# Kernel tuning notes

Hardware: AMD Instinct MI355X
Metric: run time of the kernel (lower is better)

## Reference

```python
import jax, jax.numpy as jnp
import numpy as np

N_NODES = 50000
N_EDGES = 800000
DIM = 128
NUM_GRAPHS = 512
NEG_SLOPE_ATT = 0.2   # GATConv attention leaky_relu slope
NEG_SLOPE_ACT = 0.01  # F.leaky_relu default in forward
EPS = 1e-16


def setup_inputs() -> dict:
    key = jax.random.key(0)
    ks = jax.random.split(key, 10)
    x = jax.random.normal(ks[0], (N_NODES, DIM), dtype=jnp.float32)
    edge_index = jax.random.randint(ks[1], (2, N_EDGES), 0, N_NODES, dtype=jnp.int64)
    batch = jnp.sort(jax.random.randint(ks[2], (N_NODES,), 0, NUM_GRAPHS, dtype=jnp.int64))
    s = 1.0 / np.sqrt(DIM)
    inp = {"x": x, "edge_index": edge_index, "batch": batch}
    for i in range(3):
        inp[f"W{i}"] = jax.random.uniform(ks[3 + i], (DIM, DIM), jnp.float32, -s, s)
        a = jax.random.uniform(ks[6 + i], (2, DIM), jnp.float32, -s, s)
        inp[f"a_src{i}"] = a[0]
        inp[f"a_dst{i}"] = a[1]
    return inp


def _gat_conv(x, src, dst, W, a_src, a_dst):
    # h = lin(x); heads=1, concat, bias=False
    h = x @ W.T                                     # [N, D]
    e = jax.nn.leaky_relu((h @ a_src)[src] + (h @ a_dst)[dst], NEG_SLOPE_ATT)  # [E]
    # segment softmax over destination neighborhoods
    m = jax.ops.segment_max(e, dst, num_segments=N_NODES)
    ee = jnp.exp(e - m[dst])
    z = jax.ops.segment_sum(ee, dst, num_segments=N_NODES)
    alpha = ee / (z[dst] + EPS)                     # [E]
    return jax.ops.segment_sum(h[src] * alpha[:, None], dst, num_segments=N_NODES)


def reference(x, edge_index, batch, W0, a_src0, a_dst0, W1, a_src1, a_dst1, W2, a_src2, a_dst2):
    loops = jnp.arange(N_NODES, dtype=edge_index.dtype)
    src = jnp.concatenate([edge_index[0], loops])  # add_self_loops=True
    dst = jnp.concatenate([edge_index[1], loops])
    x = _gat_conv(x, src, dst, W0, a_src0, a_dst0)
    x = _gat_conv(x, src, dst, W1, a_src1, a_dst1)
    x = jax.nn.leaky_relu(x, NEG_SLOPE_ACT)
    x = _gat_conv(x, src, dst, W2, a_src2, a_dst2)
    # global_add_pool
    return jax.ops.segment_sum(x, batch, num_segments=NUM_GRAPHS)
```

## Files before the change

kernel.cpp:

```cpp
#include <hip/hip_runtime.h>
#include <hip/hip_bf16.h>
#include <hip/hip_fp16.h>
#include <math.h>

#define NN 50000
#define NE 800000
#define DD 128
#define NG 512
#define NSA 0.2f
#define NSB 0.01f
#define EPS 1e-16f
#define CAP 61

typedef _Float16 half8 __attribute__((ext_vector_type(8)));
typedef float    floatx4 __attribute__((ext_vector_type(4)));

__global__ void init_kernel(unsigned short* __restrict__ csr_p, float* __restrict__ out,
                            const float* __restrict__ W0, const float* __restrict__ W1,
                            const float* __restrict__ W2, __half* __restrict__ w16) {
    int i = blockIdx.x * 256 + threadIdx.x;
    if (i < NN) ((unsigned int*)csr_p)[(size_t)i << 5] = 0;
    if (i < NG * DD) out[i] = 0.f;
    if (i < 3 * DD * DD) {
        int layer = i / (DD * DD), idx = i % (DD * DD);
        const float* Ws = (layer == 0) ? W0 : (layer == 1) ? W1 : W2;
        w16[i] = __float2half(Ws[idx]);
    }
}

#define BM 64
__device__ __forceinline__ void gemm_mfma_body(
        const float* __restrict__ X, const __half* __restrict__ W16,
        const float* __restrict__ a_src, const float* __restrict__ a_dst,
        __half* __restrict__ H16, float* __restrict__ as_, float* __restrict__ ad_,
        int row0, __half (*tile)[136]) {
    int t    = threadIdx.x;
    int wave = t >> 6;
    int lane = t & 63;
    int quad = lane >> 4;
    int mrow = lane & 15;
    int gl = min(row0 + wave * 16 + mrow, NN - 1);

    half8 afrag[4];
    #pragma unroll
    for (int kc = 0; kc < 4; ++kc) {
        int k = kc * 32 + quad * 8;
        float4 u0 = *(const float4*)&X[(size_t)gl * DD + k];
        float4 u1 = *(const float4*)&X[(size_t)gl * DD + k + 4];
        half8 a;
        a[0] = (_Float16)u0.x; a[1] = (_Float16)u0.y;
        a[2] = (_Float16)u0.z; a[3] = (_Float16)u0.w;
        a[4] = (_Float16)u1.x; a[5] = (_Float16)u1.y;
        a[6] = (_Float16)u1.z; a[7] = (_Float16)u1.w;
        afrag[kc] = a;
    }

    floatx4 acc[8] = {};
    #pragma unroll
    for (int ct = 0; ct < 8; ++ct) {
        #pragma unroll
        for (int kc = 0; kc < 4; ++kc) {
            half8 b = *(const half8*)&W16[(size_t)(ct * 16 + mrow) * DD + kc * 32 + quad * 8];
            acc[ct] = __builtin_amdgcn_mfma_f32_16x16x32_f16(afrag[kc], b, acc[ct], 0, 0, 0);
        }
    }
    #pragma unroll
    for (int ct = 0; ct < 8; ++ct) {
        #pragma unroll
        for (int reg = 0; reg < 4; ++reg)
            tile[wave * 16 + quad * 4 + reg][ct * 16 + mrow] = __float2half(acc[ct][reg]);
    }
    __syncthreads();

    int tx = t & 15;
    int ty = t >> 4;
    float asv[8], adv[8];
    #pragma unroll
    for (int c = 0; c < 8; ++c) {
        asv[c] = a_src[tx * 8 + c];
        adv[c] = a_dst[tx * 8 + c];
    }
    #pragma unroll
    for (int r = 0; r < 4; ++r) {
        int row = ty * 4 + r;
        int gr = row0 + row;
        float4 raw = *(const float4*)&tile[row][tx * 8];
        const __half2* q = (const __half2*)&raw;
        float2 c01 = __half22float2(q[0]);
        float2 c23 = __half22float2(q[1]);
        float2 c45 = __half22float2(q[2]);
        float2 c67 = __half22float2(q[3]);
        float hv[8] = {c01.x, c01.y, c23.x, c23.y, c45.x, c45.y, c67.x, c67.y};
        float ps = 0.f, pd = 0.f;
        #pragma unroll
        for (int c = 0; c < 8; ++c) {
            ps += hv[c] * asv[c];
            pd += hv[c] * adv[c];
        }
        #pragma unroll
        for (int off = 8; off >= 1; off >>= 1) {
            ps += __shfl_xor(ps, off);
            pd += __shfl_xor(pd, off);
        }
        if (gr < NN) {
            if (tx == 0) { as_[gr] = ps; ad_[gr] = pd; }
            *(float4*)&H16[(size_t)gr * DD + tx * 8] = raw;
        }
    }
}

__global__ __launch_bounds__(256, 4) void fat_kernel(
        int gemm_nblocks,
        const float* __restrict__ X, const __half* __restrict__ W16,
        const float* __restrict__ a_src, const float* __restrict__ a_dst,
        __half* __restrict__ H16, float* __restrict__ as_, float* __restrict__ ad_,
        const int* __restrict__ esrc, const int* __restrict__ edst,
        unsigned short* __restrict__ csr_p) {
    __shared__ __half tile[BM][136];
    if ((int)blockIdx.x >= gemm_nblocks) {
        int i = (blockIdx.x - gemm_nblocks) * 256 + threadIdx.x;
        if (i < NE / 8) {
            int4 sa = ((const int4*)esrc)[i * 2];
            int4 sb = ((const int4*)esrc)[i * 2 + 1];
            int4 da = ((const int4*)edst)[i * 2];
            int4 db = ((const int4*)edst)[i * 2 + 1];
            int k0 = atomicAdd((unsigned int*)&csr_p[(size_t)da.x << 6], 1u);
            int k1 = atomicAdd((unsigned int*)&csr_p[(size_t)da.y << 6], 1u);
            int k2 = atomicAdd((unsigned int*)&csr_p[(size_t)da.z << 6], 1u);
            int k3 = atomicAdd((unsigned int*)&csr_p[(size_t)da.w << 6], 1u);
            int k4 = atomicAdd((unsigned int*)&csr_p[(size_t)db.x << 6], 1u);
            int k5 = atomicAdd((unsigned int*)&csr_p[(size_t)db.y << 6], 1u);
            int k6 = atomicAdd((unsigned int*)&csr_p[(size_t)db.z << 6], 1u);
            int k7 = atomicAdd((unsigned int*)&csr_p[(size_t)db.w << 6], 1u);
            if (k0 < CAP) csr_p[((size_t)da.x << 6) + 2 + k0] = (unsigned short)sa.x;
            if (k1 < CAP) csr_p[((size_t)da.y << 6) + 2 + k1] = (unsigned short)sa.y;
            if (k2 < CAP) csr_p[((size_t)da.z << 6) + 2 + k2] = (unsigned short)sa.z;
            if (k3 < CAP) csr_p[((size_t)da.w << 6) + 2 + k3] = (unsigned short)sa.w;
            if (k4 < CAP) csr_p[((size_t)db.x << 6) + 2 + k4] = (unsigned short)sb.x;
            if (k5 < CAP) csr_p[((size_t)db.y << 6) + 2 + k5] = (unsigned short)sb.y;
            if (k6 < CAP) csr_p[((size_t)db.z << 6) + 2 + k6] = (unsigned short)sb.z;
            if (k7 < CAP) csr_p[((size_t)db.w << 6) + 2 + k7] = (unsigned short)sb.w;
        }
        return;
    }
    gemm_mfma_body(X, W16, a_src, a_dst, H16, as_, ad_, blockIdx.x * BM, tile);
}

__device__ inline void xr4s(float4& a, int off) {
    a.x += __shfl_xor(a.x, off);
    a.y += __shfl_xor(a.y, off);
    a.z += __shfl_xor(a.z, off);
    a.w += __shfl_xor(a.w, off);
}
__device__ inline void fma_h8(float4& a0, float4& a1, float p, const float4& raw) {
    const __half2* q = (const __half2*)&raw;
    float2 c;
    c = __half22float2(q[0]); a0.x += p * c.x; a0.y += p * c.y;
    c = __half22float2(q[1]); a0.z += p * c.x; a0.w += p * c.y;
    c = __half22float2(q[2]); a1.x += p * c.x; a1.y += p * c.y;
    c = __half22float2(q[3]); a1.z += p * c.x; a1.w += p * c.y;
}

__device__ __forceinline__ void agg_batch4(
        int row0, int wid, int lane,
        const __half* __restrict__ H16, const float* __restrict__ as_,
        const float* __restrict__ ad_, const unsigned short* __restrict__ csr_p,
        float (*p_sh)[4][64], int (*s_sh)[4][64], __half (*ytile)[136],
        int apply_lrelu) {
    int nodes[4], deg[4], sv[4];
    float adn[4], ll[4];

    int cnt[4];
    #pragma unroll
    for (int it = 0; it < 4; ++it) {
        nodes[it] = row0 + it * 4 + wid;
        cnt[it] = (int)*(const unsigned int*)&csr_p[(size_t)nodes[it] << 6];
    }
    int sl[4];
    #pragma unroll
    for (int it = 0; it < 4; ++it)
        sl[it] = (int)csr_p[((size_t)nodes[it] << 6) + 2 + lane];
    #pragma unroll
    for (int it = 0; it < 4; ++it) adn[it] = ad_[nodes[it]];
    #pragma unroll
    for (int it = 0; it < 4; ++it) {
        int dr = min(cnt[it], CAP);
        deg[it] = dr + 1;
        sv[it] = (lane < dr) ? sl[it] : nodes[it];
        s_sh[wid][it][lane] = sv[it];
    }
    float av[4];
    #pragma unroll
    for (int it = 0; it < 4; ++it) av[it] = as_[sv[it]];
    #pragma unroll
    for (int it = 0; it < 4; ++it) {
        float e = -1e30f;
        if (lane < deg[it]) {
            float ev = av[it] + adn[it];
            e = (ev > 0.f) ? ev : NSA * ev;
        }
        float m = e;
        #pragma unroll
        for (int off = 32; off >= 1; off >>= 1) m = fmaxf(m, __shfl_xor(m, off));
        float pv = (lane < deg[it]) ? __expf(e - m) : 0.f;
        p_sh[wid][it][lane] = pv;
        float l = pv;
        #pragma unroll
        for (int off = 32; off >= 1; off >>= 1) l += __shfl_xor(l, off);
        ll[it] = l;
    }
    __builtin_amdgcn_wave_barrier();

    int g = lane >> 4;
    int d = lane & 15;
    const float4* H4 = (const float4*)H16;
    #pragma unroll
    for (int it = 0; it < 4; ++it) {
        int degp = (deg[it] + 15) & ~15;
        float4 a0 = {0,0,0,0}, a1 = {0,0,0,0};
        for (int j = g; j < degp; j += 16) {
            int   sa = s_sh[wid][it][j];
            int   sb = s_sh[wid][it][j + 4];
            int   sc = s_sh[wid][it][j + 8];
            int   sd = s_sh[wid][it][j + 12];
            float pa = p_sh[wid][it][j];
            float pb = p_sh[wid][it][j + 4];
            float pc = p_sh[wid][it][j + 8];
            float pd = p_sh[wid][it][j + 12];
            float4 ra = H4[(size_t)sa * 16 + d];
            float4 rb = H4[(size_t)sb * 16 + d];
            float4 rc = H4[(size_t)sc * 16 + d];
            float4 rd = H4[(size_t)sd * 16 + d];
            fma_h8(a0, a1, pa, ra);
            fma_h8(a0, a1, pb, rb);
            fma_h8(a0, a1, pc, rc);
            fma_h8(a0, a1, pd, rd);
        }
        xr4s(a0, 16); xr4s(a0, 32);
        xr4s(a1, 16); xr4s(a1, 32);
        if (g == 0) {
            float inv = 1.f / (ll[it] + EPS);
            float4 o0, o1;
            o0.x = a0.x * inv; o0.y = a0.y * inv; o0.z = a0.z * inv; o0.w = a0.w * inv;
            o1.x = a1.x * inv; o1.y = a1.y * inv; o1.z = a1.z * inv; o1.w = a1.w * inv;
            if (apply_lrelu) {
                o0.x = (o0.x > 0.f) ? o0.x : NSB * o0.x;
                o0.y = (o0.y > 0.f) ? o0.y : NSB * o0.y;
                o0.z = (o0.z > 0.f) ? o0.z : NSB * o0.z;
                o0.w = (o0.w > 0.f) ? o0.w : NSB * o0.w;
                o1.x = (o1.x > 0.f) ? o1.x : NSB * o1.x;
                o1.y = (o1.y > 0.f) ? o1.y : NSB * o1.y;
                o1.z = (o1.z > 0.f) ? o1.z : NSB * o1.z;
                o1.w = (o1.w > 0.f) ? o1.w : NSB * o1.w;
            }
            __half2 hh[4];
            hh[0] = __floats2half2_rn(o0.x, o0.y);
            hh[1] = __floats2half2_rn(o0.z, o0.w);
            hh[2] = __floats2half2_rn(o1.x, o1.y);
            hh[3] = __floats2half2_rn(o1.z, o1.w);
            *(float4*)&ytile[it * 4 + wid][d * 8] = *(float4*)hh;
        }
    }
}

__global__ __launch_bounds__(256, 6) void agg_gemm_kernel(
        const __half* __restrict__ H_in, const float* __restrict__ as_in,
        const float* __restrict__ ad_in, const unsigned short* __restrict__ csr_p,
        const __half* __restrict__ W16, const float* __restrict__ a_src,
        const float* __restrict__ a_dst, __half* __restrict__ H_out,
        float* __restrict__ as_out, float* __restrict__ ad_out, int apply_lrelu) {
    __shared__ float  p_sh[4][4][64];
    __shared__ int    s_sh[4][4][64];
    __shared__ __half ytile[16][136];
    int t = threadIdx.x;
    int wid = t >> 6, lane = t & 63;
    int row0 = blockIdx.x * 16;

    agg_batch4(row0, wid, lane, H_in, as_in, ad_in, csr_p, p_sh, s_sh, ytile,
               apply_lrelu);
    __syncthreads();

    int quad = lane >> 4, mrow = lane & 15;
    half8 afrag[4];
    #pragma unroll
    for (int kc = 0; kc < 4; ++kc)
        afrag[kc] = *(const half8*)&ytile[mrow][kc * 32 + quad * 8];
    __syncthreads();

    floatx4 acc[2] = {};
    #pragma unroll
    for (int cc = 0; cc < 2; ++cc) {
        int ct = wid * 2 + cc;
        #pragma unroll
        for (int kc = 0; kc < 4; ++kc) {
            half8 b = *(const half8*)&W16[(size_t)(ct * 16 + mrow) * DD + kc * 32 + quad * 8];
            acc[cc] = __builtin_amdgcn_mfma_f32_16x16x32_f16(afrag[kc], b, acc[cc], 0, 0, 0);
        }
    }
    #pragma unroll
    for (int cc = 0; cc < 2; ++cc) {
        int ct = wid * 2 + cc;
        #pragma unroll
        for (int reg = 0; reg < 4; ++reg)
            ytile[quad * 4 + reg][ct * 16 + mrow] = __float2half(acc[cc][reg]);
    }
    __syncthreads();

    int row = t >> 4, cg = t & 15;
    int gr = row0 + row;
    float4 raw = *(const float4*)&ytile[row][cg * 8];
    const __half2* q = (const __half2*)&raw;
    float2 c01 = __half22float2(q[0]);
    float2 c23 = __half22float2(q[1]);
    float2 c45 = __half22float2(q[2]);
    float2 c67 = __half22float2(q[3]);
    float hv[8] = {c01.x, c01.y, c23.x, c23.y, c45.x, c45.y, c67.x, c67.y};
    float ps = 0.f, pd = 0.f;
    #pragma unroll
    for (int c = 0; c < 8; ++c) {
        ps += hv[c] * a_src[cg * 8 + c];
        pd += hv[c] * a_dst[cg * 8 + c];
    }
    #pragma unroll
    for (int off = 8; off >= 1; off >>= 1) {
        ps += __shfl_xor(ps, off);
        pd += __shfl_xor(pd, off);
    }
    if (cg == 0) { as_out[gr] = ps; ad_out[gr] = pd; }
    *(float4*)&H_out[(size_t)gr * DD + cg * 8] = raw;
}

__global__ __launch_bounds__(256, 6) void agg_pool_kernel(
        const __half* __restrict__ H_in, const float* __restrict__ as_in,
        const float* __restrict__ ad_in, const unsigned short* __restrict__ csr_p,
        const int* __restrict__ batch, float* __restrict__ out) {
    __shared__ float  p_sh[4][4][64];
    __shared__ int    s_sh[4][4][64];
    __shared__ __half ytile[16][136];
    int t = threadIdx.x;
    int wid = t >> 6, lane = t & 63;
    int row0 = blockIdx.x * 16;

    agg_batch4(row0, wid, lane, H_in, as_in, ad_in, csr_p, p_sh, s_sh, ytile, 0);
    __syncthreads();

    int rh = t >> 7;
    int d  = t & 127;
    int r0 = rh * 8;
    float acc = 0.f;
    int g = batch[row0 + r0];
    #pragma unroll
    for (int r = 0; r < 8; ++r) {
        int n = row0 + r0 + r;
        int gn = batch[n];
        if (gn != g) {
            atomicAdd(&out[(size_t)g * DD + d], acc);
            acc = 0.f;
            g = gn;
        }
        acc += __half2float(ytile[r0 + r][d]);
    }
    atomicAdd(&out[(size_t)g * DD + d], acc);
}

extern "C" void kernel_launch(void* const* d_in, const int* in_sizes, int n_in,
                              void* d_out, int out_size, void* d_ws, size_t ws_size,
                              hipStream_t stream) {
    const float* x      = (const float*)d_in[0];
    const int*   ei     = (const int*)d_in[1];
    const int*   batch  = (const int*)d_in[2];
    const int*   src    = ei;
    const int*   dst    = ei + NE;
    float* out = (float*)d_out;

    size_t off = 0;
    auto carve = [&](size_t bytes) {
        void* p = (char*)d_ws + off;
        off += (bytes + 255) & ~(size_t)255;
        return p;
    };
    __half* h16a  = (__half*)carve((size_t)NN * DD * 2);
    __half* h16b  = (__half*)carve((size_t)NN * DD * 2);
    float*  as_a  = (float*)carve((size_t)NN * 4);
    float*  ad_a  = (float*)carve((size_t)NN * 4);
    float*  as_b  = (float*)carve((size_t)NN * 4);
    float*  ad_b  = (float*)carve((size_t)NN * 4);
    unsigned short* csr_p = (unsigned short*)carve((size_t)NN * 64 * 2);
    __half* w16   = (__half*)carve((size_t)3 * DD * DD * 2);

    const int gemm_blocks = (NN + BM - 1) / BM;
    const int scat_blocks = (NE / 8 + 255) / 256;
    const int fuse_blocks = NN / 16;
    const int init_blocks = (NN * 16 + 255) / 256;

    const float* W0  = (const float*)d_in[3];
    const float* av0 = (const float*)d_in[4];
    const float* ad0 = (const float*)d_in[5];
    const float* av1 = (const float*)d_in[7];
    const float* ad1 = (const float*)d_in[8];
    const float* av2 = (const float*)d_in[10];
    const float* ad2 = (const float*)d_in[11];

    init_kernel<<<init_blocks, 256, 0, stream>>>(csr_p, out, W0,
                                                 (const float*)d_in[6],
                                                 (const float*)d_in[9], w16);
    fat_kernel<<<gemm_blocks + scat_blocks, 256, 0, stream>>>(
        gemm_blocks, x, w16, av0, ad0, h16a, as_a, ad_a, src, dst, csr_p);

    agg_gemm_kernel<<<fuse_blocks, 256, 0, stream>>>(
        h16a, as_a, ad_a, csr_p, w16 + (size_t)1 * DD * DD, av1, ad1,
        h16b, as_b, ad_b, 0);
    agg_gemm_kernel<<<fuse_blocks, 256, 0, stream>>>(
        h16b, as_b, ad_b, csr_p, w16 + (size_t)2 * DD * DD, av2, ad2,
        h16a, as_a, ad_a, 1);

    agg_pool_kernel<<<fuse_blocks, 256, 0, stream>>>(h16a, as_a, ad_a, csr_p,
                                                     batch, out);
}
```

Baseline: 252.5 us.

## Give each 16-lane group its own node in aggregation and split CSR counters

Aggregation is reorganized so each 16-lane group of a wave processes one destination node over its whole neighbor list with 8 gathers in flight. This replaces four groups cooperating on each node and then combining partials with xor shuffles. Edge counts move out of the padded CSR rows into a separate counter array with one counter per 64 bytes. The edge scatter now handles 4 edges per thread and its blocks are interleaved with the GEMM blocks of the first kernel. Launch bounds for the aggregation kernels drop from 6 to 4. The trade-off is more load imbalance between groups whose nodes have different degrees, and possibly lower occupancy.

```diff
diff --git a/kernel.cpp b/kernel.cpp
--- a/kernel.cpp
+++ b/kernel.cpp
@@ -15,11 +15,11 @@
 typedef _Float16 half8 __attribute__((ext_vector_type(8)));
 typedef float    floatx4 __attribute__((ext_vector_type(4)));
 
-__global__ void init_kernel(unsigned short* __restrict__ csr_p, float* __restrict__ out,
+__global__ void init_kernel(unsigned int* __restrict__ cnt, float* __restrict__ out,
                             const float* __restrict__ W0, const float* __restrict__ W1,
                             const float* __restrict__ W2, __half* __restrict__ w16) {
     int i = blockIdx.x * 256 + threadIdx.x;
-    if (i < NN) ((unsigned int*)csr_p)[(size_t)i << 5] = 0;
+    if (i < NN) cnt[(size_t)i << 4] = 0u;
     if (i < NG * DD) out[i] = 0.f;
     if (i < 3 * DD * DD) {
         int layer = i / (DD * DD), idx = i % (DD * DD);
@@ -110,48 +110,32 @@
 }
 
 __global__ __launch_bounds__(256, 4) void fat_kernel(
-        int gemm_nblocks,
         const float* __restrict__ X, const __half* __restrict__ W16,
         const float* __restrict__ a_src, const float* __restrict__ a_dst,
         __half* __restrict__ H16, float* __restrict__ as_, float* __restrict__ ad_,
         const int* __restrict__ esrc, const int* __restrict__ edst,
-        unsigned short* __restrict__ csr_p) {
+        unsigned int* __restrict__ cnt, unsigned short* __restrict__ slots) {
     __shared__ __half tile[BM][136];
-    if ((int)blockIdx.x >= gemm_nblocks) {
-        int i = (blockIdx.x - gemm_nblocks) * 256 + threadIdx.x;
-        if (i < NE / 8) {
-            int4 sa = ((const int4*)esrc)[i * 2];
-            int4 sb = ((const int4*)esrc)[i * 2 + 1];
-            int4 da = ((const int4*)edst)[i * 2];
-            int4 db = ((const int4*)edst)[i * 2 + 1];
-            int k0 = atomicAdd((unsigned int*)&csr_p[(size_t)da.x << 6], 1u);
-            int k1 = atomicAdd((unsigned int*)&csr_p[(size_t)da.y << 6], 1u);
-            int k2 = atomicAdd((unsigned int*)&csr_p[(size_t)da.z << 6], 1u);
-            int k3 = atomicAdd((unsigned int*)&csr_p[(size_t)da.w << 6], 1u);
-            int k4 = atomicAdd((unsigned int*)&csr_p[(size_t)db.x << 6], 1u);
-            int k5 = atomicAdd((unsigned int*)&csr_p[(size_t)db.y << 6], 1u);
-            int k6 = atomicAdd((unsigned int*)&csr_p[(size_t)db.z << 6], 1u);
-            int k7 = atomicAdd((unsigned int*)&csr_p[(size_t)db.w << 6], 1u);
-            if (k0 < CAP) csr_p[((size_t)da.x << 6) + 2 + k0] = (unsigned short)sa.x;
-            if (k1 < CAP) csr_p[((size_t)da.y << 6) + 2 + k1] = (unsigned short)sa.y;
-            if (k2 < CAP) csr_p[((size_t)da.z << 6) + 2 + k2] = (unsigned short)sa.z;
-            if (k3 < CAP) csr_p[((size_t)da.w << 6) + 2 + k3] = (unsigned short)sa.w;
-            if (k4 < CAP) csr_p[((size_t)db.x << 6) + 2 + k4] = (unsigned short)sb.x;
-            if (k5 < CAP) csr_p[((size_t)db.y << 6) + 2 + k5] = (unsigned short)sb.y;
-            if (k6 < CAP) csr_p[((size_t)db.z << 6) + 2 + k6] = (unsigned short)sb.z;
-            if (k7 < CAP) csr_p[((size_t)db.w << 6) + 2 + k7] = (unsigned short)sb.w;
+    int bx = blockIdx.x;
+    if (bx & 1) {
+        int i = (bx >> 1) * 256 + threadIdx.x;
+        if (i < NE / 4) {
+            int4 s4 = ((const int4*)esrc)[i];
+            int4 d4 = ((const int4*)edst)[i];
+            int k0 = (int)atomicAdd(&cnt[(size_t)d4.x << 4], 1u);
+            int k1 = (int)atomicAdd(&cnt[(size_t)d4.y << 4], 1u);
+            int k2 = (int)atomicAdd(&cnt[(size_t)d4.z << 4], 1u);
+            int k3 = (int)atomicAdd(&cnt[(size_t)d4.w << 4], 1u);
+            if (k0 < CAP) slots[((size_t)d4.x << 6) + k0] = (unsigned short)s4.x;
+            if (k1 < CAP) slots[((size_t)d4.y << 6) + k1] = (unsigned short)s4.y;
+            if (k2 < CAP) slots[((size_t)d4.z << 6) + k2] = (unsigned short)s4.z;
+            if (k3 < CAP) slots[((size_t)d4.w << 6) + k3] = (unsigned short)s4.w;
         }
         return;
     }
-    gemm_mfma_body(X, W16, a_src, a_dst, H16, as_, ad_, blockIdx.x * BM, tile);
-}
-
-__device__ inline void xr4s(float4& a, int off) {
-    a.x += __shfl_xor(a.x, off);
-    a.y += __shfl_xor(a.y, off);
-    a.z += __shfl_xor(a.z, off);
-    a.w += __shfl_xor(a.w, off);
-}
+    gemm_mfma_body(X, W16, a_src, a_dst, H16, as_, ad_, (bx >> 1) * BM, tile);
+}
+
 __device__ inline void fma_h8(float4& a0, float4& a1, float p, const float4& raw) {
     const __half2* q = (const __half2*)&raw;
     float2 c;
@@ -164,34 +148,36 @@
 __device__ __forceinline__ void agg_batch4(
         int row0, int wid, int lane,
         const __half* __restrict__ H16, const float* __restrict__ as_,
-        const float* __restrict__ ad_, const unsigned short* __restrict__ csr_p,
+        const float* __restrict__ ad_, const unsigned int* __restrict__ cnt,
+        const unsigned short* __restrict__ slots,
         float (*p_sh)[4][64], int (*s_sh)[4][64], __half (*ytile)[136],
         int apply_lrelu) {
-    int nodes[4], deg[4], sv[4];
+    int nodes[4], deg[4];
     float adn[4], ll[4];
 
-    int cnt[4];
+    int cv[4];
     #pragma unroll
     for (int it = 0; it < 4; ++it) {
         nodes[it] = row0 + it * 4 + wid;
-        cnt[it] = (int)*(const unsigned int*)&csr_p[(size_t)nodes[it] << 6];
+        cv[it] = (int)cnt[(size_t)nodes[it] << 4];
     }
     int sl[4];
     #pragma unroll
     for (int it = 0; it < 4; ++it)
-        sl[it] = (int)csr_p[((size_t)nodes[it] << 6) + 2 + lane];
+        sl[it] = (int)slots[((size_t)nodes[it] << 6) + lane];
     #pragma unroll
     for (int it = 0; it < 4; ++it) adn[it] = ad_[nodes[it]];
+    int svv[4];
     #pragma unroll
     for (int it = 0; it < 4; ++it) {
-        int dr = min(cnt[it], CAP);
+        int dr = min(cv[it], CAP);
         deg[it] = dr + 1;
-        sv[it] = (lane < dr) ? sl[it] : nodes[it];
-        s_sh[wid][it][lane] = sv[it];
+        svv[it] = (lane < dr) ? sl[it] : nodes[it];
+        s_sh[wid][it][lane] = svv[it];
     }
     float av[4];
     #pragma unroll
-    for (int it = 0; it < 4; ++it) av[it] = as_[sv[it]];
+    for (int it = 0; it < 4; ++it) av[it] = as_[svv[it]];
     #pragma unroll
     for (int it = 0; it < 4; ++it) {
         float e = -1e30f;
@@ -213,59 +199,61 @@
 
     int g = lane >> 4;
     int d = lane & 15;
-    const float4* H4 = (const float4*)H16;
-    #pragma unroll
-    for (int it = 0; it < 4; ++it) {
-        int degp = (deg[it] + 15) & ~15;
-        float4 a0 = {0,0,0,0}, a1 = {0,0,0,0};
-        for (int j = g; j < degp; j += 16) {
-            int   sa = s_sh[wid][it][j];
-            int   sb = s_sh[wid][it][j + 4];
-            int   sc = s_sh[wid][it][j + 8];
-            int   sd = s_sh[wid][it][j + 12];
-            float pa = p_sh[wid][it][j];
-            float pb = p_sh[wid][it][j + 4];
-            float pc = p_sh[wid][it][j + 8];
-            float pd = p_sh[wid][it][j + 12];
-            float4 ra = H4[(size_t)sa * 16 + d];
-            float4 rb = H4[(size_t)sb * 16 + d];
-            float4 rc = H4[(size_t)sc * 16 + d];
-            float4 rd = H4[(size_t)sd * 16 + d];
-            fma_h8(a0, a1, pa, ra);
-            fma_h8(a0, a1, pb, rb);
-            fma_h8(a0, a1, pc, rc);
-            fma_h8(a0, a1, pd, rd);
-        }
-        xr4s(a0, 16); xr4s(a0, 32);
-        xr4s(a1, 16); xr4s(a1, 32);
-        if (g == 0) {
-            float inv = 1.f / (ll[it] + EPS);
-            float4 o0, o1;
-            o0.x = a0.x * inv; o0.y = a0.y * inv; o0.z = a0.z * inv; o0.w = a0.w * inv;
-            o1.x = a1.x * inv; o1.y = a1.y * inv; o1.z = a1.z * inv; o1.w = a1.w * inv;
-            if (apply_lrelu) {
-                o0.x = (o0.x > 0.f) ? o0.x : NSB * o0.x;
-                o0.y = (o0.y > 0.f) ? o0.y : NSB * o0.y;
-                o0.z = (o0.z > 0.f) ? o0.z : NSB * o0.z;
-                o0.w = (o0.w > 0.f) ? o0.w : NSB * o0.w;
-                o1.x = (o1.x > 0.f) ? o1.x : NSB * o1.x;
-                o1.y = (o1.y > 0.f) ? o1.y : NSB * o1.y;
-                o1.z = (o1.z > 0.f) ? o1.z : NSB * o1.z;
-                o1.w = (o1.w > 0.f) ? o1.w : NSB * o1.w;
-            }
-            __half2 hh[4];
-            hh[0] = __floats2half2_rn(o0.x, o0.y);
-            hh[1] = __floats2half2_rn(o0.z, o0.w);
-            hh[2] = __floats2half2_rn(o1.x, o1.y);
-            hh[3] = __floats2half2_rn(o1.z, o1.w);
-            *(float4*)&ytile[it * 4 + wid][d * 8] = *(float4*)hh;
-        }
-    }
-}
-
-__global__ __launch_bounds__(256, 6) void agg_gemm_kernel(
+    int   dg = (g == 0) ? deg[0] : (g == 1) ? deg[1] : (g == 2) ? deg[2] : deg[3];
+    float lg = (g == 0) ? ll[0]  : (g == 1) ? ll[1]  : (g == 2) ? ll[2]  : ll[3];
+    const int*    srow = s_sh[wid][g];
+    const float*  prow = p_sh[wid][g];
+    const float4* H4   = (const float4*)H16;
+    float4 a0 = {0,0,0,0}, a1 = {0,0,0,0};
+    int degp = (dg + 7) & ~7;
+    for (int j = 0; j < degp; j += 8) {
+        int s0 = srow[j+0], s1 = srow[j+1], s2 = srow[j+2], s3 = srow[j+3];
+        int s4 = srow[j+4], s5 = srow[j+5], s6 = srow[j+6], s7 = srow[j+7];
+        float p0 = prow[j+0], p1 = prow[j+1], p2 = prow[j+2], p3 = prow[j+3];
+        float p4 = prow[j+4], p5 = prow[j+5], p6 = prow[j+6], p7 = prow[j+7];
+        float4 r0 = H4[(size_t)s0 * 16 + d];
+        float4 r1 = H4[(size_t)s1 * 16 + d];
+        float4 r2 = H4[(size_t)s2 * 16 + d];
+        float4 r3 = H4[(size_t)s3 * 16 + d];
+        float4 r4 = H4[(size_t)s4 * 16 + d];
+        float4 r5 = H4[(size_t)s5 * 16 + d];
+        float4 r6 = H4[(size_t)s6 * 16 + d];
+        float4 r7 = H4[(size_t)s7 * 16 + d];
+        fma_h8(a0, a1, p0, r0);
+        fma_h8(a0, a1, p1, r1);
+        fma_h8(a0, a1, p2, r2);
+        fma_h8(a0, a1, p3, r3);
+        fma_h8(a0, a1, p4, r4);
+        fma_h8(a0, a1, p5, r5);
+        fma_h8(a0, a1, p6, r6);
+        fma_h8(a0, a1, p7, r7);
+    }
+    float inv = 1.f / (lg + EPS);
+    float4 o0, o1;
+    o0.x = a0.x * inv; o0.y = a0.y * inv; o0.z = a0.z * inv; o0.w = a0.w * inv;
+    o1.x = a1.x * inv; o1.y = a1.y * inv; o1.z = a1.z * inv; o1.w = a1.w * inv;
+    if (apply_lrelu) {
+        o0.x = (o0.x > 0.f) ? o0.x : NSB * o0.x;
+        o0.y = (o0.y > 0.f) ? o0.y : NSB * o0.y;
+        o0.z = (o0.z > 0.f) ? o0.z : NSB * o0.z;
+        o0.w = (o0.w > 0.f) ? o0.w : NSB * o0.w;
+        o1.x = (o1.x > 0.f) ? o1.x : NSB * o1.x;
+        o1.y = (o1.y > 0.f) ? o1.y : NSB * o1.y;
+        o1.z = (o1.z > 0.f) ? o1.z : NSB * o1.z;
+        o1.w = (o1.w > 0.f) ? o1.w : NSB * o1.w;
+    }
+    __half2 hh[4];
+    hh[0] = __floats2half2_rn(o0.x, o0.y);
+    hh[1] = __floats2half2_rn(o0.z, o0.w);
+    hh[2] = __floats2half2_rn(o1.x, o1.y);
+    hh[3] = __floats2half2_rn(o1.z, o1.w);
+    *(float4*)&ytile[g * 4 + wid][d * 8] = *(float4*)hh;
+}
+
+__global__ __launch_bounds__(256, 4) void agg_gemm_kernel(
         const __half* __restrict__ H_in, const float* __restrict__ as_in,
-        const float* __restrict__ ad_in, const unsigned short* __restrict__ csr_p,
+        const float* __restrict__ ad_in, const unsigned int* __restrict__ cnt,
+        const unsigned short* __restrict__ slots,
         const __half* __restrict__ W16, const float* __restrict__ a_src,
         const float* __restrict__ a_dst, __half* __restrict__ H_out,
         float* __restrict__ as_out, float* __restrict__ ad_out, int apply_lrelu) {
@@ -276,7 +264,7 @@
     int wid = t >> 6, lane = t & 63;
     int row0 = blockIdx.x * 16;
 
-    agg_batch4(row0, wid, lane, H_in, as_in, ad_in, csr_p, p_sh, s_sh, ytile,
+    agg_batch4(row0, wid, lane, H_in, as_in, ad_in, cnt, slots, p_sh, s_sh, ytile,
                apply_lrelu);
     __syncthreads();
 
@@ -330,9 +318,10 @@
     *(float4*)&H_out[(size_t)gr * DD + cg * 8] = raw;
 }
 
-__global__ __launch_bounds__(256, 6) void agg_pool_kernel(
+__global__ __launch_bounds__(256, 4) void agg_pool_kernel(
         const __half* __restrict__ H_in, const float* __restrict__ as_in,
-        const float* __restrict__ ad_in, const unsigned short* __restrict__ csr_p,
+        const float* __restrict__ ad_in, const unsigned int* __restrict__ cnt,
+        const unsigned short* __restrict__ slots,
         const int* __restrict__ batch, float* __restrict__ out) {
     __shared__ float  p_sh[4][4][64];
     __shared__ int    s_sh[4][4][64];
@@ -341,7 +330,7 @@
     int wid = t >> 6, lane = t & 63;
     int row0 = blockIdx.x * 16;
 
-    agg_batch4(row0, wid, lane, H_in, as_in, ad_in, csr_p, p_sh, s_sh, ytile, 0);
+    agg_batch4(row0, wid, lane, H_in, as_in, ad_in, cnt, slots, p_sh, s_sh, ytile, 0);
     __syncthreads();
 
     int rh = t >> 7;
@@ -385,13 +374,14 @@
     float*  ad_a  = (float*)carve((size_t)NN * 4);
     float*  as_b  = (float*)carve((size_t)NN * 4);
     float*  ad_b  = (float*)carve((size_t)NN * 4);
-    unsigned short* csr_p = (unsigned short*)carve((size_t)NN * 64 * 2);
+    unsigned int*   cnt   = (unsigned int*)carve((size_t)NN * 16 * 4);
+    unsigned short* slots = (unsigned short*)carve((size_t)NN * 64 * 2);
     __half* w16   = (__half*)carve((size_t)3 * DD * DD * 2);
 
     const int gemm_blocks = (NN + BM - 1) / BM;
-    const int scat_blocks = (NE / 8 + 255) / 256;
+    const int fat_blocks  = gemm_blocks * 2;
     const int fuse_blocks = NN / 16;
-    const int init_blocks = (NN * 16 + 255) / 256;
+    const int init_blocks = (NG * DD + 255) / 256;
 
     const float* W0  = (const float*)d_in[3];
     const float* av0 = (const float*)d_in[4];
@@ -401,19 +391,19 @@
     const float* av2 = (const float*)d_in[10];
     const float* ad2 = (const float*)d_in[11];
 
-    init_kernel<<<init_blocks, 256, 0, stream>>>(csr_p, out, W0,
+    init_kernel<<<init_blocks, 256, 0, stream>>>(cnt, out, W0,
                                                  (const float*)d_in[6],
                                                  (const float*)d_in[9], w16);
-    fat_kernel<<<gemm_blocks + scat_blocks, 256, 0, stream>>>(
-        gemm_blocks, x, w16, av0, ad0, h16a, as_a, ad_a, src, dst, csr_p);
+    fat_kernel<<<fat_blocks, 256, 0, stream>>>(
+        x, w16, av0, ad0, h16a, as_a, ad_a, src, dst, cnt, slots);
 
     agg_gemm_kernel<<<fuse_blocks, 256, 0, stream>>>(
-        h16a, as_a, ad_a, csr_p, w16 + (size_t)1 * DD * DD, av1, ad1,
+        h16a, as_a, ad_a, cnt, slots, w16 + (size_t)1 * DD * DD, av1, ad1,
         h16b, as_b, ad_b, 0);
     agg_gemm_kernel<<<fuse_blocks, 256, 0, stream>>>(
-        h16b, as_b, ad_b, csr_p, w16 + (size_t)2 * DD * DD, av2, ad2,
+        h16b, as_b, ad_b, cnt, slots, w16 + (size_t)2 * DD * DD, av2, ad2,
         h16a, as_a, ad_a, 1);
 
-    agg_pool_kernel<<<fuse_blocks, 256, 0, stream>>>(h16a, as_a, ad_a, csr_p,
+    agg_pool_kernel<<<fuse_blocks, 256, 0, stream>>>(h16a, as_a, ad_a, cnt, slots,
                                                      batch, out);
 }
```

Result: faster. 246.4 us (-2.4%).
